# Optimization experiments

Measured on AMD Instinct MI355X. Metric: run time of the kernel, lower is better.

## Reference

```python
import jax, jax.numpy as jnp
import numpy as np

N_NODES = 100000
N_EDGES = 1250000
D = 64


def setup_inputs() -> dict:
    key = jax.random.key(0)
    ks = jax.random.split(key, 5)
    x = jax.random.normal(ks[0], (N_NODES, D), dtype=jnp.float32)
    edge_index = jax.random.randint(ks[1], (2, N_EDGES), 0, N_NODES, dtype=jnp.int64)
    # Linear weights stored as [in, out] so y = x @ W + b
    scale = 1.0 / np.sqrt(D)
    W1 = jax.random.normal(ks[2], (D, D), dtype=jnp.float32) * scale
    b1 = jnp.zeros((D,), dtype=jnp.float32)
    W2 = jax.random.normal(ks[3], (D, D), dtype=jnp.float32) * scale
    b2 = jnp.zeros((D,), dtype=jnp.float32)
    return {"x": x, "edge_index": edge_index, "W1": W1, "b1": b1, "W2": W2, "b2": b2}


def reference(x, edge_index, W1, b1, W2, b2):
    # GINConv with default eps=0: h_i = MLP((1+eps)*x_i + sum_{j in N(i)} x_j)
    src, dst = edge_index[0], edge_index[1]
    # gather source features, scatter-add into destination nodes
    agg = jax.ops.segment_sum(x[src], dst, num_segments=x.shape[0])  # [N, D]
    h = x + agg  # (1 + eps) * x + agg, eps = 0
    # 2-layer MLP: Linear -> ReLU -> Linear
    h = jax.nn.relu(h @ W1 + b1)
    return h @ W2 + b2
```

## Files before the change

### kernel.cpp

```cpp
#include <hip/hip_runtime.h>

#define D 64
#define SCAN_CHUNK 1024
#define NXCD 8
#define NPB 192
#define NBMAX 1024
#define CAP 4096
#define ECHUNK 4096
#define EPB (ECHUNK / 256)
#define HSTR 72
#define DEGMAX 64
#define DEGSTR 65

typedef unsigned short ushort_t;
typedef __bf16 bf16_t;
typedef __bf16 bf16x8 __attribute__((ext_vector_type(8)));
typedef float f32x4 __attribute__((ext_vector_type(4)));
typedef ushort_t ushort8 __attribute__((ext_vector_type(8)));

__device__ __forceinline__ ushort_t f2bf(float v) {
    unsigned u = __float_as_uint(v);
    return (ushort_t)((u + 0x7FFF + ((u >> 16) & 1)) >> 16);
}
__device__ __forceinline__ float bf2f(ushort_t h) {
    return __uint_as_float((unsigned)h << 16);
}


__global__ __launch_bounds__(256) void sort_cast_kernel(const int* __restrict__ src,
                                                        const int* __restrict__ dst,
                                                        int* __restrict__ gcnt,
                                                        uint2* __restrict__ buf,
                                                        const float4* __restrict__ x4,
                                                        ushort4* __restrict__ xh4,
                                                        int n4,
                                                        const float* __restrict__ W1,
                                                        const float* __restrict__ W2,
                                                        ushort_t* __restrict__ w1t,
                                                        ushort_t* __restrict__ w2t,
                                                        int nEdges, int nB, int cap,
                                                        int nSortB, int nCastB) {
    __shared__ uint2 sp[ECHUNK];
    __shared__ int lhist[NBMAX];
    __shared__ int lofs[NBMAX];
    __shared__ int lbase[NBMAX];
    __shared__ int lcur[NBMAX];
    __shared__ int wsum[4];

    int tid = threadIdx.x;

    if (blockIdx.x >= nSortB) {
        int cb = blockIdx.x - nSortB;
        if (cb == nCastB) {
#pragma unroll
            for (int i = 0; i < 16; i++) {
                int idx = i * 256 + tid;
                int k = idx >> 6, n = idx & 63;
                w1t[n * 64 + k] = f2bf(W1[idx]);
                w2t[n * 64 + k] = f2bf(W2[idx]);
            }
            return;
        }
        int gid = cb * 512 + tid;
        if (gid < n4) {
            float4 v = x4[gid];
            ushort4 o;
            o.x = f2bf(v.x); o.y = f2bf(v.y); o.z = f2bf(v.z); o.w = f2bf(v.w);
            xh4[gid] = o;
        }
        int gid2 = gid + 256;
        if (gid2 < n4) {
            float4 v = x4[gid2];
            ushort4 o;
            o.x = f2bf(v.x); o.y = f2bf(v.y); o.z = f2bf(v.z); o.w = f2bf(v.w);
            xh4[gid2] = o;
        }
        return;
    }

    int lane = tid & 63;
    int wave = tid >> 6;
    int e0 = blockIdx.x * ECHUNK;
    int cnt = min(ECHUNK, nEdges - e0);

    for (int i = tid; i < nB; i += 256) lhist[i] = 0;
    __syncthreads();

    int es[EPB], ed[EPB];
#pragma unroll
    for (int j = 0; j < EPB; j++) {
        int ii = tid + j * 256;
        if (ii < cnt) {
            es[j] = src[e0 + ii];
            ed[j] = dst[e0 + ii];
            atomicAdd(&lhist[ed[j] / NPB], 1);
        } else {
            ed[j] = -1;
        }
    }
    __syncthreads();

    int G = (nB + 255) / 256;
    int b0 = tid * G;
    int tsum = 0;
    for (int j = 0; j < G; j++) {
        int b = b0 + j;
        if (b < nB) tsum += lhist[b];
    }
    int incl = tsum;
#pragma unroll
    for (int dd = 1; dd < 64; dd <<= 1) {
        int t2 = __shfl_up(incl, dd, 64);
        if (lane >= dd) incl += t2;
    }
    if (lane == 63) wsum[wave] = incl;
    __syncthreads();
    int wo = 0;
#pragma unroll
    for (int w = 0; w < 4; w++)
        if (w < wave) wo += wsum[w];
    int run = wo + incl - tsum;
    for (int j = 0; j < G; j++) {
        int b = b0 + j;
        if (b < nB) {
            int h = lhist[b];
            lofs[b] = run;
            lcur[b] = run;
            if (h > 0) lbase[b] = atomicAdd(&gcnt[b], h);
            run += h;
        }
    }
    __syncthreads();

#pragma unroll
    for (int j = 0; j < EPB; j++) {
        if (ed[j] >= 0) {
            int b = ed[j] / NPB;
            int p = atomicAdd(&lcur[b], 1);
            sp[p] = make_uint2((unsigned)es[j], (unsigned)ed[j]);
        }
    }
    __syncthreads();

    for (int i = tid; i < cnt; i += 256) {
        uint2 pr = sp[i];
        int b = (int)pr.y / NPB;
        int idx = lbase[b] + (i - lofs[b]);
        if (idx < cap) buf[(size_t)b * cap + idx] = pr;
    }
}

__global__ __launch_bounds__(256) void csr_agg_mlp_kernel(const ushort_t* __restrict__ xh,
                                                          const uint2* __restrict__ buf,
                                                          const int* __restrict__ gcnt,
                                                          const ushort_t* __restrict__ w1t,
                                                          const ushort_t* __restrict__ w2t,
                                                          const float* __restrict__ b1,
                                                          const float* __restrict__ b2,
                                                          float* __restrict__ out,
                                                          int nNodes) {
    __shared__ int ssort[64 * DEGSTR];
    __shared__ int deg[64];
    __shared__ ushort_t ht[4][16 * HSTR];

    int tid = threadIdx.x;
    int base = blockIdx.x * 64;
    int bkt = base / NPB;
    int blo = bkt * NPB;

    if (tid < 64) deg[tid] = 0;
    __syncthreads();
    {
        int cnt = min(gcnt[bkt], CAP);
        const uint2* bp = buf + (size_t)bkt * CAP;
        for (int i = tid; i < cnt; i += 256) {
            uint2 pr = bp[i];
            int r = (int)pr.y - base;
            if ((unsigned)r < 64u) {
                int p = atomicAdd(&deg[r], 1);
                if (p < DEGMAX) ssort[r * DEGSTR + p] = (int)pr.x;
            }
        }
        (void)blo;
    }
    __syncthreads();

    {
        int nl = tid >> 2;
        int q = tid & 3;
        int n = min(base + nl, nNodes - 1);
        int f = q * 16;
        const ushort_t* xr = xh + (size_t)n * D + f;

        float acc[16];
        ushort8 sv0 = *(const ushort8*)(xr);
        ushort8 sv1 = *(const ushort8*)(xr + 8);
#pragma unroll
        for (int j = 0; j < 8; j++) {
            acc[j] = bf2f(sv0[j]);
            acc[8 + j] = bf2f(sv1[j]);
        }

        int dg = min(deg[nl], DEGMAX);
        const int* el = ssort + nl * DEGSTR;
        int e = 0;
        for (; e + 2 <= dg; e += 2) {
            int s0 = el[e];
            int s1 = el[e + 1];
            const ushort_t* p0 = xh + (size_t)s0 * D + f;
            const ushort_t* p1 = xh + (size_t)s1 * D + f;
            ushort8 a0 = *(const ushort8*)(p0);
            ushort8 b0 = *(const ushort8*)(p0 + 8);
            ushort8 a1 = *(const ushort8*)(p1);
            ushort8 b1v = *(const ushort8*)(p1 + 8);
#pragma unroll
            for (int j = 0; j < 8; j++) {
                acc[j] += bf2f(a0[j]) + bf2f(a1[j]);
                acc[8 + j] += bf2f(b0[j]) + bf2f(b1v[j]);
            }
        }
        if (e < dg) {
            int s = el[e];
            const ushort_t* p = xh + (size_t)s * D + f;
            ushort8 a = *(const ushort8*)(p);
            ushort8 bb = *(const ushort8*)(p + 8);
#pragma unroll
            for (int j = 0; j < 8; j++) {
                acc[j] += bf2f(a[j]);
                acc[8 + j] += bf2f(bb[j]);
            }
        }

        ushort8 o0, o1;
#pragma unroll
        for (int j = 0; j < 8; j++) {
            o0[j] = f2bf(acc[j]);
            o1[j] = f2bf(acc[8 + j]);
        }
        ushort_t* hr = ht[tid >> 6] + (nl & 15) * HSTR + f;
        *(ushort8*)(hr) = o0;
        *(ushort8*)(hr + 8) = o1;
    }

    int lane = tid & 63;
    int wave = tid >> 6;
    int quad = lane >> 4;
    int col = lane & 15;

    bf16x8 w1f[4][2], w2f[4][2];
#pragma unroll
    for (int nt = 0; nt < 4; nt++)
#pragma unroll
        for (int ks = 0; ks < 2; ks++) {
            int nn = nt * 16 + col;
            w1f[nt][ks] = *(const bf16x8*)(w1t + nn * 64 + ks * 32 + quad * 8);
            w2f[nt][ks] = *(const bf16x8*)(w2t + nn * 64 + ks * 32 + quad * 8);
        }
    float bb1[4], bb2[4];
#pragma unroll
    for (int nt = 0; nt < 4; nt++) {
        bb1[nt] = b1[nt * 16 + col];
        bb2[nt] = b2[nt * 16 + col];
    }

    ushort_t* tw = ht[wave];
    bf16x8 a0 = *(const bf16x8*)(tw + col * HSTR + quad * 8);
    bf16x8 a1 = *(const bf16x8*)(tw + col * HSTR + 32 + quad * 8);

    f32x4 c;
#pragma unroll
    for (int nt = 0; nt < 4; nt++) {
        c = (f32x4){0.f, 0.f, 0.f, 0.f};
        c = __builtin_amdgcn_mfma_f32_16x16x32_bf16(a0, w1f[nt][0], c, 0, 0, 0);
        c = __builtin_amdgcn_mfma_f32_16x16x32_bf16(a1, w1f[nt][1], c, 0, 0, 0);
#pragma unroll
        for (int r = 0; r < 4; r++) {
            float v = fmaxf(c[r] + bb1[nt], 0.0f);
            int m = quad * 4 + r;
            tw[m * HSTR + nt * 16 + col] = f2bf(v);
        }
    }
    bf16x8 d0 = *(const bf16x8*)(tw + col * HSTR + quad * 8);
    bf16x8 d1 = *(const bf16x8*)(tw + col * HSTR + 32 + quad * 8);
#pragma unroll
    for (int nt = 0; nt < 4; nt++) {
        c = (f32x4){0.f, 0.f, 0.f, 0.f};
        c = __builtin_amdgcn_mfma_f32_16x16x32_bf16(d0, w2f[nt][0], c, 0, 0, 0);
        c = __builtin_amdgcn_mfma_f32_16x16x32_bf16(d1, w2f[nt][1], c, 0, 0, 0);
#pragma unroll
        for (int r = 0; r < 4; r++) {
            int row = base + wave * 16 + quad * 4 + r;
            if (row < nNodes) out[(size_t)row * D + nt * 16 + col] = c[r] + bb2[nt];
        }
    }
}

__global__ __launch_bounds__(256) void zero_kernel(int* __restrict__ p, int n) {
    int gid = blockIdx.x * 256 + threadIdx.x;
    if (gid < n) p[gid] = 0;
}

__global__ __launch_bounds__(256) void hist_xcd_kernel(const int* __restrict__ dst,
                                                       int* __restrict__ counts,
                                                       int nEdges, int nNodes,
                                                       int blocksPerXcd) {
    int xcd = blockIdx.x % NXCD;
    int slice = blockIdx.x / NXCD;
    int lo = (int)((long long)nNodes * xcd / NXCD);
    int hi = (int)((long long)nNodes * (xcd + 1) / NXCD);
    int per = (nEdges + blocksPerXcd - 1) / blocksPerXcd;
    int e0 = slice * per;
    int e1 = min(e0 + per, nEdges);
    for (int e = e0 + (int)threadIdx.x; e < e1; e += 256) {
        int d = dst[e];
        if (d >= lo && d < hi) atomicAdd(&counts[d], 1);
    }
}

__global__ __launch_bounds__(256) void scan_reduce_kernel(const int* __restrict__ counts,
                                                          int* __restrict__ blockSums,
                                                          int nNodes) {
    __shared__ int ws[4];
    int base = blockIdx.x * SCAN_CHUNK;
    int tid = threadIdx.x;
    int s = 0;
#pragma unroll
    for (int i = 0; i < 4; i++) {
        int idx = base + tid + 256 * i;
        if (idx < nNodes) s += counts[idx];
    }
#pragma unroll
    for (int d = 32; d > 0; d >>= 1) s += __shfl_xor(s, d, 64);
    if ((tid & 63) == 0) ws[tid >> 6] = s;
    __syncthreads();
    if (tid == 0) blockSums[blockIdx.x] = ws[0] + ws[1] + ws[2] + ws[3];
}

__global__ __launch_bounds__(256) void scan_sums_kernel(int* __restrict__ blockSums,
                                                        int* __restrict__ off,
                                                        int nSB, int nNodes, int nEdges) {
    __shared__ int ws[4];
    int tid = threadIdx.x;
    int lane = tid & 63;
    int wave = tid >> 6;
    int v = (tid < nSB) ? blockSums[tid] : 0;
    int incl = v;
#pragma unroll
    for (int d = 1; d < 64; d <<= 1) {
        int t = __shfl_up(incl, d, 64);
        if (lane >= d) incl += t;
    }
    if (lane == 63) ws[wave] = incl;
    __syncthreads();
    int waveOff = 0;
#pragma unroll
    for (int w = 0; w < 4; w++)
        if (w < wave) waveOff += ws[w];
    if (tid < nSB) blockSums[tid] = waveOff + incl - v;
    if (tid == 0) off[nNodes] = nEdges;
}

__global__ __launch_bounds__(1024) void scan_write_kernel(int* __restrict__ off,
                                                          int* __restrict__ cur,
                                                          const int* __restrict__ blockSums,
                                                          int nNodes) {
    __shared__ int waveSums[16];
    int tid = threadIdx.x;
    int lane = tid & 63;
    int wave = tid >> 6;
    int i = blockIdx.x * SCAN_CHUNK + tid;
    int v = (i < nNodes) ? off[i] : 0;
    int incl = v;
#pragma unroll
    for (int d = 1; d < 64; d <<= 1) {
        int t = __shfl_up(incl, d, 64);
        if (lane >= d) incl += t;
    }
    if (lane == 63) waveSums[wave] = incl;
    __syncthreads();
    if (wave == 0) {
        int wv = (lane < 16) ? waveSums[lane] : 0;
        int s = wv;
#pragma unroll
        for (int d = 1; d < 16; d <<= 1) {
            int t = __shfl_up(s, d, 64);
            if (lane >= d) s += t;
        }
        if (lane < 16) waveSums[lane] = s - wv;
    }
    __syncthreads();
    if (i < nNodes) {
        int excl = blockSums[blockIdx.x] + waveSums[wave] + incl - v;
        off[i] = excl;
        cur[i] = excl;
    }
}

__global__ __launch_bounds__(256) void fill_xcd_kernel(const int* __restrict__ src,
                                                       const int* __restrict__ dst,
                                                       int* __restrict__ cur,
                                                       int* __restrict__ ssrc,
                                                       int nEdges, int nNodes,
                                                       int blocksPerXcd) {
    int xcd = blockIdx.x % NXCD;
    int slice = blockIdx.x / NXCD;
    int lo = (int)((long long)nNodes * xcd / NXCD);
    int hi = (int)((long long)nNodes * (xcd + 1) / NXCD);
    int per = (nEdges + blocksPerXcd - 1) / blocksPerXcd;
    int e0 = slice * per;
    int e1 = min(e0 + per, nEdges);
    for (int e = e0 + (int)threadIdx.x; e < e1; e += 256) {
        int d = dst[e];
        if (d >= lo && d < hi) {
            int p = atomicAdd(&cur[d], 1);
            ssrc[p] = src[e];
        }
    }
}

__global__ __launch_bounds__(256) void aggregate_kernel(const float* __restrict__ x,
                                                        const int* __restrict__ off,
                                                        const int* __restrict__ ssrc,
                                                        float* __restrict__ out,
                                                        int nNodes) {
    int gid = blockIdx.x * 256 + threadIdx.x;
    int n = gid >> 4;
    if (n >= nNodes) return;
    int f = (gid & 15) * 4;
    float4 acc = *(const float4*)(x + (size_t)n * D + f);
    int e0 = off[n], e1 = off[n + 1];
    for (int e = e0; e < e1; e++) {
        int s = ssrc[e];
        float4 v = *(const float4*)(x + (size_t)s * D + f);
        acc.x += v.x; acc.y += v.y; acc.z += v.z; acc.w += v.w;
    }
    *(float4*)(out + (size_t)n * D + f) = acc;
}

__global__ __launch_bounds__(256) void mlp_reg_kernel(const float* hin,
                                                      const float* __restrict__ W1,
                                                      const float* __restrict__ b1,
                                                      const float* __restrict__ W2,
                                                      const float* __restrict__ b2,
                                                      float* out,
                                                      int nNodes) {
    int lane = threadIdx.x & 63;
    int wave = threadIdx.x >> 6;
    float w1[D], w2[D];
#pragma unroll
    for (int k = 0; k < D; k++) w1[k] = W1[k * D + lane];
#pragma unroll
    for (int k = 0; k < D; k++) w2[k] = W2[k * D + lane];
    float bb1 = b1[lane];
    float bb2 = b2[lane];
    int gw = blockIdx.x * 4 + wave;
    int nW = gridDim.x * 4;
    for (int n = gw; n < nNodes; n += nW) {
        float hv = hin[(size_t)n * D + lane];
        float a0 = bb1, a1 = 0.0f, a2 = 0.0f, a3 = 0.0f;
#pragma unroll
        for (int k = 0; k < D; k += 4) {
            float h0 = __uint_as_float(__builtin_amdgcn_readlane(__float_as_uint(hv), k + 0));
            float h1 = __uint_as_float(__builtin_amdgcn_readlane(__float_as_uint(hv), k + 1));
            float h2 = __uint_as_float(__builtin_amdgcn_readlane(__float_as_uint(hv), k + 2));
            float h3 = __uint_as_float(__builtin_amdgcn_readlane(__float_as_uint(hv), k + 3));
            a0 = fmaf(h0, w1[k + 0], a0);
            a1 = fmaf(h1, w1[k + 1], a1);
            a2 = fmaf(h2, w1[k + 2], a2);
            a3 = fmaf(h3, w1[k + 3], a3);
        }
        float m = fmaxf((a0 + a1) + (a2 + a3), 0.0f);
        float c0 = bb2, c1 = 0.0f, c2 = 0.0f, c3 = 0.0f;
#pragma unroll
        for (int k = 0; k < D; k += 4) {
            float h0 = __uint_as_float(__builtin_amdgcn_readlane(__float_as_uint(m), k + 0));
            float h1 = __uint_as_float(__builtin_amdgcn_readlane(__float_as_uint(m), k + 1));
            float h2 = __uint_as_float(__builtin_amdgcn_readlane(__float_as_uint(m), k + 2));
            float h3 = __uint_as_float(__builtin_amdgcn_readlane(__float_as_uint(m), k + 3));
            c0 = fmaf(h0, w2[k + 0], c0);
            c1 = fmaf(h1, w2[k + 1], c1);
            c2 = fmaf(h2, w2[k + 2], c2);
            c3 = fmaf(h3, w2[k + 3], c3);
        }
        out[(size_t)n * D + lane] = (c0 + c1) + (c2 + c3);
    }
}

extern "C" void kernel_launch(void* const* d_in, const int* in_sizes, int n_in,
                              void* d_out, int out_size, void* d_ws, size_t ws_size,
                              hipStream_t stream) {
    const float* x  = (const float*)d_in[0];
    const int*   ei = (const int*)d_in[1];
    const float* W1 = (const float*)d_in[2];
    const float* b1 = (const float*)d_in[3];
    const float* W2 = (const float*)d_in[4];
    const float* b2 = (const float*)d_in[5];
    float* out = (float*)d_out;

    const int nNodes = in_sizes[0] / D;
    const int nEdges = in_sizes[1] / 2;
    const int* src = ei;
    const int* dst = ei + nEdges;

    const int NB = (nNodes + NPB - 1) / NPB;

    int* gcnt = (int*)d_ws;
    uint2* buf = (uint2*)(gcnt + 1024);
    ushort_t* xh  = (ushort_t*)(buf + (size_t)NB * CAP);
    ushort_t* w1t = xh + (size_t)nNodes * D;
    ushort_t* w2t = w1t + 4096;

    size_t wsT0 = (size_t)1024 * 4
                + (size_t)NB * CAP * 8
                + (size_t)nNodes * D * 2 + 2 * 4096 * 2;
    bool tier0 = (ws_size >= wsT0) && (NB <= NBMAX) && (nNodes > 0)
              && ((long long)nEdges * NPB / nNodes * 14 / 10 < CAP)
              && ((long long)nEdges * 2 / nNodes < DEGMAX);

    if (tier0) {
        int n4 = nNodes * (D / 4);
        int nSortB = (nEdges + ECHUNK - 1) / ECHUNK;
        int nCastB = (n4 + 511) / 512;
        hipMemsetAsync(gcnt, 0, 1024 * sizeof(int), stream);
        sort_cast_kernel<<<nSortB + nCastB + 1, 256, 0, stream>>>(
            src, dst, gcnt, buf, (const float4*)x, (ushort4*)xh, n4,
            W1, W2, w1t, w2t, nEdges, NB, CAP, nSortB, nCastB);
        int nG = (nNodes + 63) / 64;
        csr_agg_mlp_kernel<<<nG, 256, 0, stream>>>(
            xh, buf, gcnt, w1t, w2t, b1, b2, out, nNodes);
        return;
    }

    const int nSB = (nNodes + SCAN_CHUNK - 1) / SCAN_CHUNK;
    int* foff  = (int*)d_ws;
    int* fcur  = foff + (nNodes + 1);
    int* fssrc = fcur + nNodes;
    int* fsums = fssrc + nEdges;

    zero_kernel<<<(nNodes + 1 + 255) / 256, 256, 0, stream>>>(foff, nNodes + 1);
    {
        const int blocksPerXcd = 256;
        hist_xcd_kernel<<<blocksPerXcd * NXCD, 256, 0, stream>>>(
            dst, foff, nEdges, nNodes, blocksPerXcd);
    }
    scan_reduce_kernel<<<nSB, 256, 0, stream>>>(foff, fsums, nNodes);
    scan_sums_kernel<<<1, 256, 0, stream>>>(fsums, foff, nSB, nNodes, nEdges);
    scan_write_kernel<<<nSB, 1024, 0, stream>>>(foff, fcur, fsums, nNodes);
    {
        const int blocksPerXcd = 256;
        fill_xcd_kernel<<<blocksPerXcd * NXCD, 256, 0, stream>>>(
            src, dst, fcur, fssrc, nEdges, nNodes, blocksPerXcd);
    }
    long long work = (long long)nNodes * 16;
    aggregate_kernel<<<(int)((work + 255) / 256), 256, 0, stream>>>(x, foff, fssrc, out, nNodes);
    mlp_reg_kernel<<<6250, 256, 0, stream>>>(out, W1, b1, W2, b2, out, nNodes);
}
```

Before: 158.8 us.

## Pack bucketed edges into 32-bit words and unroll neighbor gather by four

Bucketed edge pairs are now stored as one 32-bit word: a 24-bit source index plus an 8-bit destination offset within the bucket. This halves the write traffic in the sort kernel and the read traffic in the aggregation kernel. The aggregation kernel reads the packed bucket with 16-byte vector loads, and the neighbor gather loop is unrolled to four edges so more loads are in flight. A guard restricts the fast path to graphs with fewer than 2^24 nodes.

Result: faster. 149.3 us (-5.9%).

```diff
diff --git a/kernel.cpp b/kernel.cpp
--- a/kernel.cpp
+++ b/kernel.cpp
@@ -30,7 +30,7 @@
 __global__ __launch_bounds__(256) void sort_cast_kernel(const int* __restrict__ src,
                                                         const int* __restrict__ dst,
                                                         int* __restrict__ gcnt,
-                                                        uint2* __restrict__ buf,
+                                                        unsigned* __restrict__ buf,
                                                         const float4* __restrict__ x4,
                                                         ushort4* __restrict__ xh4,
                                                         int n4,
@@ -146,12 +146,13 @@
         uint2 pr = sp[i];
         int b = (int)pr.y / NPB;
         int idx = lbase[b] + (i - lofs[b]);
-        if (idx < cap) buf[(size_t)b * cap + idx] = pr;
+        unsigned pk = pr.x | ((pr.y - (unsigned)b * NPB) << 24);
+        if (idx < cap) buf[(size_t)b * cap + idx] = pk;
     }
 }
 
 __global__ __launch_bounds__(256) void csr_agg_mlp_kernel(const ushort_t* __restrict__ xh,
-                                                          const uint2* __restrict__ buf,
+                                                          const unsigned* __restrict__ buf,
                                                           const int* __restrict__ gcnt,
                                                           const ushort_t* __restrict__ w1t,
                                                           const ushort_t* __restrict__ w2t,
@@ -167,21 +168,34 @@
     int base = blockIdx.x * 64;
     int bkt = base / NPB;
     int blo = bkt * NPB;
+    int roff = blo - base;
 
     if (tid < 64) deg[tid] = 0;
     __syncthreads();
     {
         int cnt = min(gcnt[bkt], CAP);
-        const uint2* bp = buf + (size_t)bkt * CAP;
-        for (int i = tid; i < cnt; i += 256) {
-            uint2 pr = bp[i];
-            int r = (int)pr.y - base;
+        const unsigned* bp = buf + (size_t)bkt * CAP;
+        int cnt4 = cnt & ~3;
+        for (int i = tid * 4; i < cnt4; i += 1024) {
+            uint4 v4 = *(const uint4*)(bp + i);
+#pragma unroll
+            for (int k = 0; k < 4; k++) {
+                unsigned v = (&v4.x)[k];
+                int r = (int)(v >> 24) + roff;
+                if ((unsigned)r < 64u) {
+                    int p = atomicAdd(&deg[r], 1);
+                    if (p < DEGMAX) ssort[r * DEGSTR + p] = (int)(v & 0xFFFFFFu);
+                }
+            }
+        }
+        if (tid < (cnt - cnt4)) {
+            unsigned v = bp[cnt4 + tid];
+            int r = (int)(v >> 24) + roff;
             if ((unsigned)r < 64u) {
                 int p = atomicAdd(&deg[r], 1);
-                if (p < DEGMAX) ssort[r * DEGSTR + p] = (int)pr.x;
+                if (p < DEGMAX) ssort[r * DEGSTR + p] = (int)(v & 0xFFFFFFu);
             }
         }
-        (void)blo;
     }
     __syncthreads();
 
@@ -204,6 +218,29 @@
         int dg = min(deg[nl], DEGMAX);
         const int* el = ssort + nl * DEGSTR;
         int e = 0;
+        for (; e + 4 <= dg; e += 4) {
+            int s0 = el[e];
+            int s1 = el[e + 1];
+            int s2 = el[e + 2];
+            int s3 = el[e + 3];
+            const ushort_t* p0 = xh + (size_t)s0 * D + f;
+            const ushort_t* p1 = xh + (size_t)s1 * D + f;
+            const ushort_t* p2 = xh + (size_t)s2 * D + f;
+            const ushort_t* p3 = xh + (size_t)s3 * D + f;
+            ushort8 a0 = *(const ushort8*)(p0);
+            ushort8 a0b = *(const ushort8*)(p0 + 8);
+            ushort8 a1 = *(const ushort8*)(p1);
+            ushort8 a1b = *(const ushort8*)(p1 + 8);
+            ushort8 a2 = *(const ushort8*)(p2);
+            ushort8 a2b = *(const ushort8*)(p2 + 8);
+            ushort8 a3 = *(const ushort8*)(p3);
+            ushort8 a3b = *(const ushort8*)(p3 + 8);
+#pragma unroll
+            for (int j = 0; j < 8; j++) {
+                acc[j]     += (bf2f(a0[j]) + bf2f(a1[j])) + (bf2f(a2[j]) + bf2f(a3[j]));
+                acc[8 + j] += (bf2f(a0b[j]) + bf2f(a1b[j])) + (bf2f(a2b[j]) + bf2f(a3b[j]));
+            }
+        }
         for (; e + 2 <= dg; e += 2) {
             int s0 = el[e];
             int s1 = el[e + 1];
@@ -505,15 +542,16 @@
     const int NB = (nNodes + NPB - 1) / NPB;
 
     int* gcnt = (int*)d_ws;
-    uint2* buf = (uint2*)(gcnt + 1024);
+    unsigned* buf = (unsigned*)(gcnt + 1024);
     ushort_t* xh  = (ushort_t*)(buf + (size_t)NB * CAP);
     ushort_t* w1t = xh + (size_t)nNodes * D;
     ushort_t* w2t = w1t + 4096;
 
     size_t wsT0 = (size_t)1024 * 4
-                + (size_t)NB * CAP * 8
+                + (size_t)NB * CAP * 4
                 + (size_t)nNodes * D * 2 + 2 * 4096 * 2;
     bool tier0 = (ws_size >= wsT0) && (NB <= NBMAX) && (nNodes > 0)
+              && (nNodes < (1 << 24))
               && ((long long)nEdges * NPB / nNodes * 14 / 10 < CAP)
               && ((long long)nEdges * 2 / nNodes < DEGMAX);
 
```
